# Kernel optimization log

Hardware: AMD Instinct MI355X
Metric: run time of the kernel (lower is better)

The kernel has to match this reference:

```python
import jax, jax.numpy as jnp
import numpy as np

H = 16        # num attention heads (TP shard)
NOPE = 128    # qk_nope_head_dim
ROPE = 64     # qk_rope_head_dim
VDIM = 128    # v_head_dim
RANK = 512    # kv_lora_rank
QIN = 1536    # q_lora_rank (input dim of q_proj)
HID = 7168    # model hidden size (o_proj output)
T = 2048      # prefill tokens
SCALE = (NOPE + ROPE) ** -0.5


def setup_inputs() -> dict:
    key = jax.random.key(0)
    ks = jax.random.split(key, 6)
    q = jax.random.normal(ks[0], (T, QIN), jnp.float32)
    k_c_normed = jax.random.normal(ks[1], (T, RANK), jnp.float32)
    k_pe = jax.random.normal(ks[2], (T, ROPE), jnp.float32)
    positions = jnp.arange(T, dtype=jnp.int32)
    # learned weights (torch Linear layout: [out, in]), variance-scaled
    wq = jax.random.normal(ks[3], (H * (NOPE + ROPE), QIN), jnp.float32) * QIN ** -0.5
    kv_b_weight = jax.random.normal(ks[4], (H * (NOPE + VDIM), RANK), jnp.float32) * RANK ** -0.5
    wo = jax.random.normal(ks[5], (HID, H * VDIM), jnp.float32) * (H * VDIM) ** -0.5
    # neox-style rope caches: [max_pos, rotary_dim/2]
    inv_freq = 1.0 / (10000.0 ** (jnp.arange(0, ROPE, 2, dtype=jnp.float32) / ROPE))
    ang = jnp.arange(T, dtype=jnp.float32)[:, None] * inv_freq[None, :]
    return dict(q=q, k_c_normed=k_c_normed, k_pe=k_pe, positions=positions,
                wq=wq, kv_b_weight=kv_b_weight, wo=wo,
                cos_cache=jnp.cos(ang), sin_cache=jnp.sin(ang))


def _rope_neox(x, cos, sin):
    # rotate-halves (neox) rope; cos/sin broadcast over head dim
    x1, x2 = jnp.split(x, 2, axis=-1)
    return jnp.concatenate([x1 * cos - x2 * sin, x2 * cos + x1 * sin], axis=-1)


def reference(q, k_c_normed, k_pe, positions, wq, kv_b_weight, wo, cos_cache, sin_cache):
    Tq = q.shape[0]
    # q projection: [T, H*(nope+rope)] -> [T, H, 192]
    qf = (q @ wq.T).reshape(Tq, H, NOPE + ROPE)
    q_nope, q_pe = qf[..., :NOPE], qf[..., NOPE:]
    cos = cos_cache[positions]
    sin = sin_cache[positions]
    q_pe = _rope_neox(q_pe, cos[:, None, :], sin[:, None, :])   # [T, H, 64]
    k_pe_r = _rope_neox(k_pe, cos, sin)                          # [T, 64] shared across heads
    # kv_b_proj weight absorption: W_UK [R, H, nope], W_UV [R, H, v]
    wkv = kv_b_weight.T.reshape(RANK, H, NOPE + VDIM)
    w_uk, w_uv = wkv[..., :NOPE], wkv[..., NOPE:]
    # absorb W_UK into queries -> query in kv-latent space [T, H, R]
    q_lat = jnp.einsum('thd,rhd->thr', q_nope, w_uk)
    # attention scores in latent space + rope part; causal mask
    scores = (jnp.einsum('thr,sr->ths', q_lat, k_c_normed)
              + jnp.einsum('thd,sd->ths', q_pe, k_pe_r)) * SCALE
    causal = positions[:, None] >= positions[None, :]            # [T, S]
    scores = jnp.where(causal[:, None, :], scores, -jnp.inf)
    attn = jax.nn.softmax(scores, axis=-1)
    # attend over latent kv, then absorb W_UV out
    o_lat = jnp.einsum('ths,sr->thr', attn, k_c_normed)
    o = jnp.einsum('thr,rhv->thv', o_lat, w_uv).reshape(Tq, H * VDIM)
    return o @ wo.T  # [T, HID]
```

## Files before the change

### kernel.cpp

```cpp
#include <hip/hip_runtime.h>

#define T_SEQ 2048
#define NH    16
#define D_NOPE 128
#define D_ROPE 64
#define D_V   128
#define RANK  512
#define D_QIN 1536
#define D_HID 7168
#define D_QK  576
#define QF_N  3072
#define ATT_SCALE 0.07216878364870322f

typedef float  f32x4  __attribute__((ext_vector_type(4)));
typedef __bf16 bf16x8 __attribute__((ext_vector_type(8)));

__device__ __forceinline__ unsigned short f2bf(float x){
  union{float f; unsigned u;} v; v.f = x;
  return (unsigned short)((v.u + 0x7fffu + ((v.u >> 16) & 1u)) >> 16);
}
__device__ __forceinline__ float bf2f(unsigned short b){
  union{unsigned u; float f;} v; v.u = ((unsigned)b) << 16; return v.f;
}
__device__ __forceinline__ bf16x8 ld_frag(const unsigned short* p){
  union{ uint4 u; bf16x8 v; } w; w.u = *(const uint4*)p; return w.v;
}
__device__ __forceinline__ void gload_lds16(const unsigned short* g, unsigned short* l){
  __builtin_amdgcn_global_load_lds(
      (const __attribute__((address_space(1))) unsigned int*)g,
      (__attribute__((address_space(3))) unsigned int*)l, 16, 0, 0);
}

__global__ void cvt_bf16_kernel(const float* __restrict__ in, unsigned short* __restrict__ out, long n){
  long i = ((long)blockIdx.x * blockDim.x + threadIdx.x) * 4;
  if (i + 3 < n){
    float4 f = *(const float4*)(in + i);
    ushort4 o; o.x = f2bf(f.x); o.y = f2bf(f.y); o.z = f2bf(f.z); o.w = f2bf(f.w);
    *(ushort4*)(out + i) = o;
  }
}

__global__ void fill_ones_kernel(unsigned short* __restrict__ p, long n){
  long i = (long)blockIdx.x * blockDim.x + threadIdx.x;
  if (i < n) p[i] = 0x3F80;
}

__global__ void prep_kcat_kernel(const float* __restrict__ kc, const float* __restrict__ kpe,
                                 const int* __restrict__ pos, const float* __restrict__ cosc,
                                 const float* __restrict__ sinc, unsigned short* __restrict__ kcat){
  int t = blockIdx.x; int tid = threadIdx.x;
  for (int c = tid; c < RANK; c += 256)
    kcat[(long)t * D_QK + c] = f2bf(kc[(long)t * RANK + c]);
  if (tid < 32){
    int p = pos[t];
    float c = cosc[p * 32 + tid], s = sinc[p * 32 + tid];
    float x1 = kpe[(long)t * D_ROPE + tid];
    float x2 = kpe[(long)t * D_ROPE + 32 + tid];
    kcat[(long)t * D_QK + RANK + tid]      = f2bf(x1 * c - x2 * s);
    kcat[(long)t * D_QK + RANK + 32 + tid] = f2bf(x2 * c + x1 * s);
  }
}

__global__ void transpose_vt_kernel(const float* __restrict__ kc, unsigned short* __restrict__ vt){
  __shared__ unsigned short tile[64][65];
  int bi = blockIdx.x, bj = blockIdx.y, tid = threadIdx.x;
  for (int c = tid; c < 4096; c += 256){
    int i = c >> 6, j = c & 63;
    tile[i][j] = f2bf(kc[(long)(bi * 64 + i) * RANK + bj * 64 + j]);
  }
  __syncthreads();
  for (int c = tid; c < 4096; c += 256){
    int j = c >> 6, i = c & 63;
    vt[(long)(bj * 64 + j) * T_SEQ + bi * 64 + i] = tile[i][j];
  }
}

__global__ void prep_wukt_kernel(const float* __restrict__ kvb, unsigned short* __restrict__ wukt){
  __shared__ unsigned short tile[64][65];
  int h = blockIdx.x, db = blockIdx.y, rb = blockIdx.z, tid = threadIdx.x;
  for (int c = tid; c < 4096; c += 256){
    int i = c >> 6, j = c & 63;
    tile[i][j] = f2bf(kvb[(long)(h * 256 + db * 64 + i) * RANK + rb * 64 + j]);
  }
  __syncthreads();
  for (int c = tid; c < 4096; c += 256){
    int j = c >> 6, i = c & 63;
    wukt[(long)h * RANK * D_NOPE + (long)(rb * 64 + j) * D_NOPE + db * 64 + i] = tile[i][j];
  }
}

__global__ void rope_q_kernel(const unsigned short* __restrict__ qf, const int* __restrict__ pos,
                              const float* __restrict__ cosc, const float* __restrict__ sinc,
                              unsigned short* __restrict__ qcat){
  int t = blockIdx.x; int tid = threadIdx.x;
  int p = pos[t];
  for (int w = tid; w < 512; w += 256){
    int h = w >> 5, i = w & 31;
    float c = cosc[p * 32 + i], s = sinc[p * 32 + i];
    float x1 = bf2f(qf[(long)t * QF_N + h * 192 + 128 + i]);
    float x2 = bf2f(qf[(long)t * QF_N + h * 192 + 128 + 32 + i]);
    long base = (long)h * T_SEQ * D_QK + (long)t * D_QK + RANK;
    qcat[base + i]      = f2bf(x1 * c - x2 * s);
    qcat[base + 32 + i] = f2bf(x2 * c + x1 * s);
  }
}

template<int OUT_BF16>
__global__ __launch_bounds__(256, 2) void gemm_nt_kernel(
    const unsigned short* __restrict__ A, long lda, long sA,
    const unsigned short* __restrict__ B, long ldb, long sB,
    void* __restrict__ Cv, long ldc, long sC,
    int M, int N, int K)
{
  const int bz = blockIdx.z;
  A += (long)bz * sA;
  B += (long)bz * sB;
  const int m0 = blockIdx.x * 128;
  const int n0 = blockIdx.y * 128;
  const int tid = threadIdx.x;
  const int lane = tid & 63, wave = tid >> 6;
  const int quad = lane >> 4, l16 = lane & 15;
  const int wm = wave & 1, wn = wave >> 1;

  __shared__ __align__(16) unsigned short As[128 * 32];
  __shared__ __align__(16) unsigned short Bs[128 * 32];

  f32x4 acc[4][4];
  #pragma unroll
  for (int mt = 0; mt < 4; ++mt)
    #pragma unroll
    for (int nt = 0; nt < 4; ++nt)
      acc[mt][nt] = (f32x4){0.f, 0.f, 0.f, 0.f};

  for (int k0 = 0; k0 < K; k0 += 32){
    __syncthreads();
    #pragma unroll
    for (int i = 0; i < 2; ++i){
      int c = i * 256 + tid;
      int row = c >> 2, col = (c & 3) * 8;
      gload_lds16(A + (long)(m0 + row) * lda + k0 + col, &As[c * 8]);
      gload_lds16(B + (long)(n0 + row) * ldb + k0 + col, &Bs[c * 8]);
    }
    __syncthreads();
    bf16x8 af[4], bg[4];
    #pragma unroll
    for (int mt = 0; mt < 4; ++mt) af[mt] = ld_frag(&As[(wm * 64 + mt * 16 + l16) * 32 + quad * 8]);
    #pragma unroll
    for (int nt = 0; nt < 4; ++nt) bg[nt] = ld_frag(&Bs[(wn * 64 + nt * 16 + l16) * 32 + quad * 8]);
    #pragma unroll
    for (int mt = 0; mt < 4; ++mt)
      #pragma unroll
      for (int nt = 0; nt < 4; ++nt)
        acc[mt][nt] = __builtin_amdgcn_mfma_f32_16x16x32_bf16(af[mt], bg[nt], acc[mt][nt], 0, 0, 0);
  }

  if (OUT_BF16){
    unsigned short* C = (unsigned short*)Cv + (long)bz * sC;
    #pragma unroll
    for (int mt = 0; mt < 4; ++mt)
      #pragma unroll
      for (int nt = 0; nt < 4; ++nt)
        #pragma unroll
        for (int r = 0; r < 4; ++r)
          C[(long)(m0 + wm * 64 + mt * 16 + quad * 4 + r) * ldc + n0 + wn * 64 + nt * 16 + l16] =
              f2bf(acc[mt][nt][r]);
  } else {
    float* C = (float*)Cv + (long)bz * sC;
    #pragma unroll
    for (int mt = 0; mt < 4; ++mt)
      #pragma unroll
      for (int nt = 0; nt < 4; ++nt)
        #pragma unroll
        for (int r = 0; r < 4; ++r)
          C[(long)(m0 + wm * 64 + mt * 16 + quad * 4 + r) * ldc + n0 + wn * 64 + nt * 16 + l16] =
              acc[mt][nt][r];
  }
}

__global__ __launch_bounds__(256, 2) void attn_kernel(
    const unsigned short* __restrict__ qcat,
    const unsigned short* __restrict__ kcat,
    const unsigned short* __restrict__ vt,
    unsigned short* __restrict__ olat)
{
  const int h = blockIdx.x;
  const int ti = (int)gridDim.y - 1 - (int)blockIdx.y;
  const int vz = blockIdx.z;
  const int t0 = ti * 64;
  const int tid = threadIdx.x;
  const int lane = tid & 63, wave = tid >> 6;
  const int quad = lane >> 4, l16 = lane & 15;
  const int t0w = t0 + wave * 16;

  __shared__ __align__(16) unsigned short Ks[2][32 * 576];
  __shared__ __align__(16) unsigned short Pw[4][16 * 40];

  const unsigned short* vbase = vt + (long)(vz * 256) * T_SEQ;
  const unsigned short* vones = vt + (long)RANK * T_SEQ;

  int goffK[9];
  #pragma unroll
  for (int i = 0; i < 9; ++i){
    int fc = i * 256 + tid;
    int r = fc / 72, u = fc - r * 72;
    int c = (u & ~7) | ((u - r) & 7);
    goffK[i] = r * D_QK + c * 8;
  }

  bf16x8 qf[18];
  {
    const unsigned short* qrow = qcat + (long)h * T_SEQ * D_QK + (long)(t0w + l16) * D_QK;
    #pragma unroll
    for (int kk = 0; kk < 18; ++kk) qf[kk] = ld_frag(qrow + kk * 32 + quad * 8);
  }

  f32x4 oacc[16];
  #pragma unroll
  for (int ct = 0; ct < 16; ++ct) oacc[ct] = (f32x4){0.f, 0.f, 0.f, 0.f};
  f32x4 oacc_l = (f32x4){0.f, 0.f, 0.f, 0.f};
  float m_run[4];
  #pragma unroll
  for (int r = 0; r < 4; ++r) m_run[r] = -3e38f;

  const int niter = 2 * (ti + 1);

  #pragma unroll
  for (int i = 0; i < 9; ++i)
    gload_lds16(kcat + goffK[i], &Ks[0][(i * 256 + tid) * 8]);
  __syncthreads();

  for (int it = 0; it < niter; ++it){
    const int s0 = it * 32;
    const int cur = it & 1;

    if (it + 1 < niter){
      const unsigned short* kb = kcat + (long)(s0 + 32) * D_QK;
      #pragma unroll
      for (int i = 0; i < 9; ++i)
        gload_lds16(kb + goffK[i], &Ks[cur ^ 1][(i * 256 + tid) * 8]);
    }

    f32x4 sacc0 = (f32x4){0.f,0.f,0.f,0.f}, sacc1 = (f32x4){0.f,0.f,0.f,0.f};
    #pragma unroll
    for (int kk = 0; kk < 18; ++kk){
      const int c = kk * 4 + quad;
      const int chi = c & ~7;
      int u0 = chi | ((c + l16) & 7);
      int u1 = chi | ((c + 16 + l16) & 7);
      bf16x8 b0 = ld_frag(&Ks[cur][l16 * 576 + u0 * 8]);
      bf16x8 b1 = ld_frag(&Ks[cur][(16 + l16) * 576 + u1 * 8]);
      sacc0 = __builtin_amdgcn_mfma_f32_16x16x32_bf16(qf[kk], b0, sacc0, 0, 0, 0);
      sacc1 = __builtin_amdgcn_mfma_f32_16x16x32_bf16(qf[kk], b1, sacc1, 0, 0, 0);
    }

    float sv[2][4], mr[4];
    #pragma unroll
    for (int r = 0; r < 4; ++r){
      int row = t0w + quad * 4 + r;
      float v0 = sacc0[r] * ATT_SCALE;
      float v1 = sacc1[r] * ATT_SCALE;
      if (s0 + l16 > row)      v0 = -3e38f;
      if (s0 + 16 + l16 > row) v1 = -3e38f;
      sv[0][r] = v0; sv[1][r] = v1; mr[r] = fmaxf(v0, v1);
    }
    #pragma unroll
    for (int d = 1; d < 16; d <<= 1)
      #pragma unroll
      for (int r = 0; r < 4; ++r) mr[r] = fmaxf(mr[r], __shfl_xor(mr[r], d, 64));
    float alpha[4];
    #pragma unroll
    for (int r = 0; r < 4; ++r){
      float mn = fmaxf(m_run[r], mr[r]);
      alpha[r] = __expf(m_run[r] - mn);
      m_run[r] = mn;
      float p0 = __expf(sv[0][r] - mn);
      float p1 = __expf(sv[1][r] - mn);
      Pw[wave][(quad * 4 + r) * 40 + l16]      = f2bf(p0);
      Pw[wave][(quad * 4 + r) * 40 + 16 + l16] = f2bf(p1);
    }

    #pragma unroll
    for (int ct = 0; ct < 16; ++ct)
      #pragma unroll
      for (int r = 0; r < 4; ++r) oacc[ct][r] *= alpha[r];
    #pragma unroll
    for (int r = 0; r < 4; ++r) oacc_l[r] *= alpha[r];

    __builtin_amdgcn_s_waitcnt(0xC07F);

    bf16x8 pa = ld_frag(&Pw[wave][l16 * 40 + quad * 8]);
    #pragma unroll
    for (int ct = 0; ct < 16; ++ct){
      bf16x8 bv = ld_frag(vbase + (long)(ct * 16 + l16) * T_SEQ + s0 + quad * 8);
      oacc[ct] = __builtin_amdgcn_mfma_f32_16x16x32_bf16(pa, bv, oacc[ct], 0, 0, 0);
    }
    {
      bf16x8 bo = ld_frag(vones + s0 + quad * 8);
      oacc_l = __builtin_amdgcn_mfma_f32_16x16x32_bf16(pa, bo, oacc_l, 0, 0, 0);
    }

    __syncthreads();
  }

  float inv[4];
  #pragma unroll
  for (int r = 0; r < 4; ++r) inv[r] = 1.0f / oacc_l[r];
  #pragma unroll
  for (int ct = 0; ct < 16; ++ct)
    #pragma unroll
    for (int r = 0; r < 4; ++r){
      int row = t0w + quad * 4 + r;
      olat[(long)h * T_SEQ * RANK + (long)row * RANK + vz * 256 + ct * 16 + l16] =
          f2bf(oacc[ct][r] * inv[r]);
    }
}

extern "C" void kernel_launch(void* const* d_in, const int* in_sizes, int n_in,
                              void* d_out, int out_size, void* d_ws, size_t ws_size,
                              hipStream_t stream){
  const float* q    = (const float*)d_in[0];
  const float* kc   = (const float*)d_in[1];
  const float* kpe  = (const float*)d_in[2];
  const int*   pos  = (const int*)d_in[3];
  const float* wq   = (const float*)d_in[4];
  const float* kvb  = (const float*)d_in[5];
  const float* wo   = (const float*)d_in[6];
  const float* cosc = (const float*)d_in[7];
  const float* sinc = (const float*)d_in[8];
  float* out = (float*)d_out;

  char* ws = (char*)d_ws;
  size_t off = 0;
  auto alloc_us = [&](long nelem) -> unsigned short* {
    unsigned short* p = (unsigned short*)(ws + off);
    off += ((size_t)nelem * 2 + 255) & ~(size_t)255;
    return p;
  };
  unsigned short* q_bf   = alloc_us((long)T_SEQ * D_QIN);
  unsigned short* wq_bf  = alloc_us((long)QF_N * D_QIN);
  unsigned short* kvb_bf = alloc_us((long)NH * 256 * RANK);
  unsigned short* wukt   = alloc_us((long)NH * RANK * D_NOPE);
  unsigned short* wo_bf  = alloc_us((long)D_HID * NH * D_V);
  unsigned short* kcat   = alloc_us((long)T_SEQ * D_QK);
  unsigned short* vt     = alloc_us((long)(RANK + 1) * T_SEQ);
  unsigned short* qf_bf  = alloc_us((long)T_SEQ * QF_N);
  unsigned short* qcat   = alloc_us((long)NH * T_SEQ * D_QK);
  unsigned short* olat   = alloc_us((long)NH * T_SEQ * RANK);
  unsigned short* o_mid  = alloc_us((long)T_SEQ * NH * D_V);

  {
    long n;
    n = (long)T_SEQ * D_QIN;
    cvt_bf16_kernel<<<dim3((unsigned)(n / 1024)), 256, 0, stream>>>(q, q_bf, n);
    n = (long)QF_N * D_QIN;
    cvt_bf16_kernel<<<dim3((unsigned)(n / 1024)), 256, 0, stream>>>(wq, wq_bf, n);
    n = (long)NH * 256 * RANK;
    cvt_bf16_kernel<<<dim3((unsigned)(n / 1024)), 256, 0, stream>>>(kvb, kvb_bf, n);
    n = (long)D_HID * NH * D_V;
    cvt_bf16_kernel<<<dim3((unsigned)(n / 1024)), 256, 0, stream>>>(wo, wo_bf, n);
  }
  prep_kcat_kernel<<<dim3(T_SEQ), 256, 0, stream>>>(kc, kpe, pos, cosc, sinc, kcat);
  transpose_vt_kernel<<<dim3(T_SEQ / 64, RANK / 64), 256, 0, stream>>>(kc, vt);
  fill_ones_kernel<<<dim3(T_SEQ / 256), 256, 0, stream>>>(vt + (long)RANK * T_SEQ, T_SEQ);
  prep_wukt_kernel<<<dim3(NH, D_NOPE / 64, RANK / 64), 256, 0, stream>>>(kvb, wukt);

  gemm_nt_kernel<1><<<dim3(T_SEQ / 128, QF_N / 128), 256, 0, stream>>>(
      q_bf, D_QIN, 0, wq_bf, D_QIN, 0, (void*)qf_bf, QF_N, 0, T_SEQ, QF_N, D_QIN);

  rope_q_kernel<<<dim3(T_SEQ), 256, 0, stream>>>(qf_bf, pos, cosc, sinc, qcat);

  gemm_nt_kernel<1><<<dim3(T_SEQ / 128, RANK / 128, NH), 256, 0, stream>>>(
      qf_bf, QF_N, 192,
      wukt, D_NOPE, (long)RANK * D_NOPE,
      (void*)qcat, D_QK, (long)T_SEQ * D_QK,
      T_SEQ, RANK, D_NOPE);

  attn_kernel<<<dim3(NH, T_SEQ / 64, 2), 256, 0, stream>>>(qcat, kcat, vt, olat);

  gemm_nt_kernel<1><<<dim3(T_SEQ / 128, D_V / 128, NH), 256, 0, stream>>>(
      olat, RANK, (long)T_SEQ * RANK,
      kvb_bf + (long)128 * RANK, RANK, (long)256 * RANK,
      (void*)o_mid, (long)NH * D_V, (long)D_V,
      T_SEQ, D_V, RANK);

  gemm_nt_kernel<0><<<dim3(T_SEQ / 128, D_HID / 128), 256, 0, stream>>>(
      o_mid, (long)NH * D_V, 0, wo_bf, (long)NH * D_V, 0, (void*)out, D_HID, 0,
      T_SEQ, D_HID, (long)NH * D_V);
}
```

Before: 655.0 us.

## Pre-swizzle K in global memory and single-buffer K tile for higher occupancy

The prep kernel now writes kcat already in the LDS swizzle order, so the attention kernel can copy K tiles linearly and no longer keeps per-thread offset registers. The K staging buffer in shared memory drops from double to single, and the launch bound rises to three blocks per SM to use the freed LDS and registers. The next tile's load is issued only after a barrier that follows the score MMAs, so it now overlaps only the softmax/PV phase, not the QK compute. That adds a sync per iteration and exposes more load latency in exchange for occupancy.

```diff
diff --git a/kernel.cpp b/kernel.cpp
--- a/kernel.cpp
+++ b/kernel.cpp
@@ -30,6 +30,11 @@
       (const __attribute__((address_space(1))) unsigned int*)g,
       (__attribute__((address_space(3))) unsigned int*)l, 16, 0, 0);
 }
+__device__ __forceinline__ int kswz(int e, int t){
+  int c = e >> 3, r = t & 31;
+  int u = (c & ~7) | ((c + r) & 7);
+  return u * 8 + (e & 7);
+}
 
 __global__ void cvt_bf16_kernel(const float* __restrict__ in, unsigned short* __restrict__ out, long n){
   long i = ((long)blockIdx.x * blockDim.x + threadIdx.x) * 4;
@@ -49,15 +54,15 @@
                                  const int* __restrict__ pos, const float* __restrict__ cosc,
                                  const float* __restrict__ sinc, unsigned short* __restrict__ kcat){
   int t = blockIdx.x; int tid = threadIdx.x;
-  for (int c = tid; c < RANK; c += 256)
-    kcat[(long)t * D_QK + c] = f2bf(kc[(long)t * RANK + c]);
+  for (int e = tid; e < RANK; e += 256)
+    kcat[(long)t * D_QK + kswz(e, t)] = f2bf(kc[(long)t * RANK + e]);
   if (tid < 32){
     int p = pos[t];
     float c = cosc[p * 32 + tid], s = sinc[p * 32 + tid];
     float x1 = kpe[(long)t * D_ROPE + tid];
     float x2 = kpe[(long)t * D_ROPE + 32 + tid];
-    kcat[(long)t * D_QK + RANK + tid]      = f2bf(x1 * c - x2 * s);
-    kcat[(long)t * D_QK + RANK + 32 + tid] = f2bf(x2 * c + x1 * s);
+    kcat[(long)t * D_QK + kswz(RANK + tid, t)]      = f2bf(x1 * c - x2 * s);
+    kcat[(long)t * D_QK + kswz(RANK + 32 + tid, t)] = f2bf(x2 * c + x1 * s);
   }
 }
 
@@ -177,7 +182,7 @@
   }
 }
 
-__global__ __launch_bounds__(256, 2) void attn_kernel(
+__global__ __launch_bounds__(256, 3) void attn_kernel(
     const unsigned short* __restrict__ qcat,
     const unsigned short* __restrict__ kcat,
     const unsigned short* __restrict__ vt,
@@ -192,20 +197,11 @@
   const int quad = lane >> 4, l16 = lane & 15;
   const int t0w = t0 + wave * 16;
 
-  __shared__ __align__(16) unsigned short Ks[2][32 * 576];
+  __shared__ __align__(16) unsigned short Ks[32 * 576];
   __shared__ __align__(16) unsigned short Pw[4][16 * 40];
 
   const unsigned short* vbase = vt + (long)(vz * 256) * T_SEQ;
   const unsigned short* vones = vt + (long)RANK * T_SEQ;
-
-  int goffK[9];
-  #pragma unroll
-  for (int i = 0; i < 9; ++i){
-    int fc = i * 256 + tid;
-    int r = fc / 72, u = fc - r * 72;
-    int c = (u & ~7) | ((u - r) & 7);
-    goffK[i] = r * D_QK + c * 8;
-  }
 
   bf16x8 qf[18];
   {
@@ -226,19 +222,11 @@
 
   #pragma unroll
   for (int i = 0; i < 9; ++i)
-    gload_lds16(kcat + goffK[i], &Ks[0][(i * 256 + tid) * 8]);
+    gload_lds16(kcat + (long)(i * 256 + tid) * 8, &Ks[(i * 256 + tid) * 8]);
   __syncthreads();
 
   for (int it = 0; it < niter; ++it){
     const int s0 = it * 32;
-    const int cur = it & 1;
-
-    if (it + 1 < niter){
-      const unsigned short* kb = kcat + (long)(s0 + 32) * D_QK;
-      #pragma unroll
-      for (int i = 0; i < 9; ++i)
-        gload_lds16(kb + goffK[i], &Ks[cur ^ 1][(i * 256 + tid) * 8]);
-    }
 
     f32x4 sacc0 = (f32x4){0.f,0.f,0.f,0.f}, sacc1 = (f32x4){0.f,0.f,0.f,0.f};
     #pragma unroll
@@ -247,10 +235,18 @@
       const int chi = c & ~7;
       int u0 = chi | ((c + l16) & 7);
       int u1 = chi | ((c + 16 + l16) & 7);
-      bf16x8 b0 = ld_frag(&Ks[cur][l16 * 576 + u0 * 8]);
-      bf16x8 b1 = ld_frag(&Ks[cur][(16 + l16) * 576 + u1 * 8]);
+      bf16x8 b0 = ld_frag(&Ks[l16 * 576 + u0 * 8]);
+      bf16x8 b1 = ld_frag(&Ks[(16 + l16) * 576 + u1 * 8]);
       sacc0 = __builtin_amdgcn_mfma_f32_16x16x32_bf16(qf[kk], b0, sacc0, 0, 0, 0);
       sacc1 = __builtin_amdgcn_mfma_f32_16x16x32_bf16(qf[kk], b1, sacc1, 0, 0, 0);
+    }
+    __syncthreads();
+
+    if (it + 1 < niter){
+      const unsigned short* kb = kcat + (long)(s0 + 32) * D_QK;
+      #pragma unroll
+      for (int i = 0; i < 9; ++i)
+        gload_lds16(kb + (long)(i * 256 + tid) * 8, &Ks[(i * 256 + tid) * 8]);
     }
 
     float sv[2][4], mr[4];
```

Measured after the change: 839.6 us. 28.2% more time.
